# Kernel optimization log

Measured on AMD Instinct MI355X. Metric: run time of the kernel, lower is better.

Reference implementation:

```python
import jax, jax.numpy as jnp
import numpy as np

ATOM_DIM = 128; RBF_DIM = 32; GEOM_HID = 128; SCAT = 64; OUT = 64; CUTOFF = 5.0
MAX_Z = 100; Z_EMB = 32; E_DIM = 32; PAIR_HID = 64
B = 16; N = 64; P = 8000; NE = 80


def _lin(key, i, o):
    kw, kb = jax.random.split(key)
    W = jax.random.normal(kw, (i, o), jnp.float32) / np.sqrt(i).astype(np.float32)
    b = jax.random.normal(kb, (o,), jnp.float32) * 0.01
    return W, b


def setup_inputs() -> dict:
    key = jax.random.key(0)
    ks = jax.random.split(key, 24)
    inp = {}
    inp["h_flat"] = jax.random.normal(ks[0], (B * N, ATOM_DIM), jnp.float32)
    inp["z_flat"] = jax.random.randint(ks[1], (B * N,), 0, MAX_Z + 1)
    inp["e_feat"] = jax.random.normal(ks[2], (NE, E_DIM), jnp.float32)
    inp["path_j"] = jax.random.randint(ks[3], (P,), 0, B * N)
    inp["path_k"] = jax.random.randint(ks[4], (P,), 0, B * N)
    # distances in (0, 1.2*cutoff) so some paths exceed the cutoff
    inp["path_r0j"] = jax.random.uniform(ks[5], (P,), jnp.float32, 0.1, 1.2 * CUTOFF)
    inp["path_r0k"] = jax.random.uniform(ks[6], (P,), jnp.float32, 0.1, 1.2 * CUTOFF)
    inp["path_rjk"] = jax.random.uniform(ks[7], (P,), jnp.float32, 0.1, 1.2 * CUTOFF)
    inp["path_cosangle"] = jax.random.uniform(ks[8], (P,), jnp.float32, -1.0, 1.0)
    inp["path_batch"] = jnp.sort(jax.random.randint(ks[9], (P,), 0, B))
    inp["bsz"] = B
    # params
    inp["z_emb"] = jax.random.normal(ks[10], (MAX_Z + 1, Z_EMB), jnp.float32)
    pe_in = 2 * Z_EMB + E_DIM
    inp["pe_w1"], inp["pe_b1"] = _lin(ks[11], pe_in, PAIR_HID)
    inp["pe_w2"], inp["pe_b2"] = _lin(ks[12], PAIR_HID, PAIR_HID)
    inp["pe_w3"], inp["pe_b3"] = _lin(ks[13], PAIR_HID, SCAT)
    gm_in = 2 * ATOM_DIM + 3 * RBF_DIM + 1
    inp["gm_w1"], inp["gm_b1"] = _lin(ks[14], gm_in, GEOM_HID)
    inp["gm_w2"], inp["gm_b2"] = _lin(ks[15], GEOM_HID, GEOM_HID)
    inp["gm_w3"], inp["gm_b3"] = _lin(ks[16], GEOM_HID, SCAT)
    inp["op_w1"], inp["op_b1"] = _lin(ks[17], SCAT, GEOM_HID)
    inp["op_w2"], inp["op_b2"] = _lin(ks[18], GEOM_HID, OUT)
    return inp


def _rbf(r):
    centers = jnp.linspace(0.0, CUTOFF, RBF_DIM)
    width = centers[1] - centers[0]
    return jnp.exp(-0.5 * ((r[..., None] - centers) / width) ** 2)


def _cutoff_fn(r):
    return 0.5 * (jnp.cos(jnp.pi * r / CUTOFF) + 1.0) * (r < CUTOFF)


def _mlp3(x, w1, b1, w2, b2, w3, b3):
    h = jax.nn.silu(x @ w1 + b1)
    h = jax.nn.silu(h @ w2 + b2)
    return h @ w3 + b3


def _mlp2(x, w1, b1, w2, b2):
    return jax.nn.silu(x @ w1 + b1) @ w2 + b2


def reference(h_flat, z_flat, e_feat, path_j, path_k, path_r0j, path_r0k,
              path_rjk, path_cosangle, path_batch, bsz, z_emb,
              pe_w1, pe_b1, pe_w2, pe_b2, pe_w3, pe_b3,
              gm_w1, gm_b1, gm_w2, gm_b2, gm_w3, gm_b3,
              op_w1, op_b1, op_w2, op_b2):
    n_e = e_feat.shape[0]
    n_p = path_j.shape[0]
    # gather atom features
    hj = h_flat[path_j]                                  # (P, atom_dim)
    hk = h_flat[path_k]
    f0j = _rbf(jnp.minimum(path_r0j, CUTOFF))            # (P, rbf_dim)
    f0k = _rbf(jnp.minimum(path_r0k, CUTOFF))
    fjk = _rbf(jnp.minimum(path_rjk, CUTOFF))
    geom_in = jnp.concatenate([hj, hk, f0j, f0k, fjk, path_cosangle[:, None]], axis=-1)
    g_geom = _mlp3(geom_in, gm_w1, gm_b1, gm_w2, gm_b2, gm_w3, gm_b3)  # (P, scat)
    # element-pair energy features
    ej = z_emb[z_flat[path_j]]                           # (P, z_emb)
    ek = z_emb[z_flat[path_k]]
    pair_in = jnp.concatenate([
        jnp.broadcast_to(ej[:, None, :], (n_p, n_e, ej.shape[-1])),
        jnp.broadcast_to(ek[:, None, :], (n_p, n_e, ek.shape[-1])),
        jnp.broadcast_to(e_feat[None, :, :], (n_p, n_e, e_feat.shape[-1])),
    ], axis=-1)                                          # (P, nE, 2*z_emb+e_dim)
    g_elem = _mlp3(pair_in, pe_w1, pe_b1, pe_w2, pe_b2, pe_w3, pe_b3)  # (P, nE, scat)
    # cutoff weights and outer-product contribution
    cw = _cutoff_fn(path_r0j) * _cutoff_fn(path_r0k) * _cutoff_fn(path_rjk)  # (P,)
    contrib = g_geom[:, None, :] * g_elem * cw[:, None, None]          # (P, nE, scat)
    # scatter-add into batch bins
    agg = jax.ops.segment_sum(contrib, path_batch, num_segments=bsz)   # (B, nE, scat)
    norm = jax.ops.segment_sum(cw, path_batch, num_segments=bsz)       # (B,)
    agg = agg / jnp.maximum(norm, 1e-8)[:, None, None]
    return _mlp2(agg, op_w1, op_b1, op_w2, op_b2)                      # (B, nE, out)
```

## Files before the change

### kernel.cpp

```cpp
#include <hip/hip_runtime.h>
#include <math.h>

typedef float f32x4 __attribute__((ext_vector_type(4)));
typedef short bf16x8 __attribute__((ext_vector_type(8)));
typedef unsigned short u16;

#define RBF_DIM 32
#define CUTOFF 5.0f
#define PI_F 3.14159265358979323846f
#define BB 16
#define PP 8000
#define NEE 80

#define CW_OFF      0
#define GCW_OFF     8000
#define AGG_OFF     520000
#define ZEJW_OFF    601920
#define ZEKW_OFF    608384
#define EFWB_OFF    614848
#define NORM_OFF    619968
#define AIDX_OFF    619984
#define ZJA_OFF     627984
#define ZKA_OFF     635984
#define BOFF_OFF    643984
#define BCNT_OFF    644004
#define BSUM_OFF    644036
#define BCNTB_OFF   644548
#define BLKOFF_OFF  645060
#define CHS_OFF     645096
#define CHC_OFF     645362
#define CHB_OFF     645628
#define NC_OFF      645894
#define W2THI_OFF   645896
#define W2TLO_OFF   647944
#define W3THI_OFF   649992
#define W3TLO_OFF   652040
#define PJA_OFF     654088
#define PKA_OFF     662088
#define CWA_OFF     670088
#define HHI_OFF     678088
#define HLO_OFF     743624
#define GW1JKH_OFF  809160
#define GW1JKL_OFF  825544
#define GW1RH_OFF   841928
#define GW1RL_OFF   850120
#define GW2H_OFF    858312
#define GW2L_OFF    866504
#define GW3H_OFF    874696
#define GW3L_OFF    878792
#define HJW_OFF     882888
#define HKW_OFF     1013960

__device__ __forceinline__ float siluf(float x) { return x / (1.f + __expf(-x)); }
__device__ __forceinline__ float cutoff_fn(float r) {
    return (r < CUTOFF) ? 0.5f * (cosf(PI_F * r / CUTOFF) + 1.f) : 0.f;
}
__device__ __forceinline__ float rbff(float r, int i) {
    r = fminf(r, CUTOFF);
    float a = r * (31.0f / CUTOFF) - (float)i;
    return __expf(-0.5f * a * a);
}
__device__ __forceinline__ u16 f2bf_rne(float x) {
    unsigned u = __float_as_uint(x);
    return (u16)((u + 0x7FFFu + ((u >> 16) & 1u)) >> 16);
}
__device__ __forceinline__ unsigned cvtpk2(float a, float b) {
    unsigned r;
    asm("v_cvt_pk_bf16_f32 %0, %1, %2" : "=v"(r) : "v"(a), "v"(b));
    return r;
}
__device__ __forceinline__ void splitpack8(const float* xs, bf16x8& hi, bf16x8& lo) {
    union { bf16x8 v; unsigned u[4]; } H, L;
    #pragma unroll
    for (int d = 0; d < 4; ++d) {
        float a = xs[2 * d], b = xs[2 * d + 1];
        unsigned h = cvtpk2(a, b);
        float ra = a - __uint_as_float(h << 16);
        float rb = b - __uint_as_float(h & 0xFFFF0000u);
        H.u[d] = h;
        L.u[d] = cvtpk2(ra, rb);
    }
    hi = H.v; lo = L.v;
}

__global__ __launch_bounds__(256) void k0a_k1(
    const float* r0j, const float* r0k, const float* rjk, const int* pbatch,
    const float* z_emb, const float* e_feat, const float* pe_w1, const float* pe_b1,
    const float* pe_w2, const float* pe_w3,
    const float* h_flat, const float* gm_w1, const float* gm_w2, const float* gm_w3,
    float* ws, int* wsi)
{
    __shared__ float cwL[256];
    __shared__ int bL[256];
    __shared__ int redC[256];
    __shared__ float embL[4 * 32];
    int blkAll = blockIdx.x, t = threadIdx.x;
    if (blkAll < 32) {
        int bi = blkAll;
        for (int i = t; i < 2560; i += 256) ws[AGG_OFF + bi*2560 + i] = 0.f;
        int p = bi*250 + t;
        float cw = 0.f; int bin = -1; int valid = 0;
        if (t < 250) {
            cw = cutoff_fn(r0j[p]) * cutoff_fn(r0k[p]) * cutoff_fn(rjk[p]);
            ws[CW_OFF + p] = cw;
            bin = pbatch[p];
            valid = (cw > 0.f) ? 1 : 0;
        }
        cwL[t] = cw; bL[t] = bin; redC[t] = valid;
        __syncthreads();
        if (t < 16) {
            float s = 0.f; int c2 = 0;
            for (int i = 0; i < 256; ++i) {
                bool m = (bL[i] == t);
                s += m ? cwL[i] : 0.f;
                c2 += (m && cwL[i] > 0.f) ? 1 : 0;
            }
            ws[BSUM_OFF + bi*16 + t] = s;
            wsi[BCNTB_OFF + bi*16 + t] = c2;
        }
        __syncthreads();
        for (int s = 128; s > 0; s >>= 1) {
            if (t < s) redC[t] += redC[t + s];
            __syncthreads();
        }
        if (t == 0) wsi[BCNT_OFF + bi] = redC[0];
        return;
    }
    if (blkAll >= 106) {
        int blk = blkAll - 106;
        if (blk < 32) {
            u16* hh = (u16*)(ws + HHI_OFF);
            u16* hl = (u16*)(ws + HLO_OFF);
            int base = blk * 4096;
            for (int idx = t; idx < 4096; idx += 256) {
                int e = base + idx;
                float v = h_flat[e];
                u16 h = f2bf_rne(v);
                hh[e] = h;
                hl[e] = f2bf_rne(v - __uint_as_float(((unsigned)h) << 16));
            }
        } else if (blk < 34) {
            u16* wh = (u16*)(ws + GW1JKH_OFF);
            u16* wl = (u16*)(ws + GW1JKL_OFF);
            int base = (blk - 32) * 16384;
            for (int idx = t; idx < 16384; idx += 256) {
                int e = base + idx;
                int m = e >> 7, k = e & 127;
                float v = gm_w1[((m < 128) ? k : (128 + k)) * 128 + (m & 127)];
                u16 h = f2bf_rne(v);
                wh[e] = h;
                wl[e] = f2bf_rne(v - __uint_as_float(((unsigned)h) << 16));
            }
        } else if (blk == 34) {
            u16* wh = (u16*)(ws + GW1RH_OFF);
            u16* wl = (u16*)(ws + GW1RL_OFF);
            for (int e = t; e < 16384; e += 256) {
                int m = e >> 7, k = e & 127;
                float v = (k < 97) ? gm_w1[(256 + k) * 128 + m] : 0.f;
                u16 h = f2bf_rne(v);
                wh[e] = h;
                wl[e] = f2bf_rne(v - __uint_as_float(((unsigned)h) << 16));
            }
        } else if (blk == 35) {
            u16* wh = (u16*)(ws + GW2H_OFF);
            u16* wl = (u16*)(ws + GW2L_OFF);
            for (int e = t; e < 16384; e += 256) {
                int m = e >> 7, k = e & 127;
                float v = gm_w2[k * 128 + m];
                u16 h = f2bf_rne(v);
                wh[e] = h;
                wl[e] = f2bf_rne(v - __uint_as_float(((unsigned)h) << 16));
            }
        } else {
            u16* wh = (u16*)(ws + GW3H_OFF);
            u16* wl = (u16*)(ws + GW3L_OFF);
            for (int e = t; e < 8192; e += 256) {
                int m = e >> 7, k = e & 127;
                float v = gm_w3[k * 64 + m];
                u16 h = f2bf_rne(v);
                wh[e] = h;
                wl[e] = f2bf_rne(v - __uint_as_float(((unsigned)h) << 16));
            }
        }
        return;
    }
    int blk = blkAll - 32;
    if (blk >= 72) {
        const float* W = (blk == 72) ? pe_w2 : pe_w3;
        u16* hiD = (u16*)(ws + ((blk == 72) ? W2THI_OFF : W3THI_OFF));
        u16* loD = (u16*)(ws + ((blk == 72) ? W2TLO_OFF : W3TLO_OFF));
        for (int idx = t; idx < 4096; idx += 256) {
            int k = idx >> 6, n = idx & 63;
            float v = W[idx];
            u16 h = f2bf_rne(v);
            float hf = __uint_as_float(((unsigned)h) << 16);
            hiD[n*64 + k] = h;
            loD[n*64 + k] = f2bf_rne(v - hf);
        }
        return;
    }
    int r0, nrows, wbase;
    const float* src;
    float* dst;
    bool addb = false;
    if (blk < 26)      { r0 = blk * 4;        nrows = 101; src = z_emb;  wbase = 0;  dst = ws + ZEJW_OFF; }
    else if (blk < 52) { r0 = (blk - 26) * 4; nrows = 101; src = z_emb;  wbase = 32; dst = ws + ZEKW_OFF; }
    else               { r0 = (blk - 52) * 4; nrows = NEE; src = e_feat; wbase = 64; dst = ws + EFWB_OFF; addb = true; }
    if (t < 128) {
        int rl = t >> 5, i = t & 31;
        int r = r0 + rl;
        embL[t] = (r < nrows) ? src[r * 32 + i] : 0.f;
    }
    __syncthreads();
    int rl = t >> 6, c = t & 63;
    float acc = addb ? pe_b1[c] : 0.f;
    #pragma unroll
    for (int i = 0; i < 32; ++i)
        acc = fmaf(embL[rl * 32 + i], pe_w1[(wbase + i) * 64 + c], acc);
    int r = r0 + rl;
    if (r < nrows) dst[r * 64 + c] = acc;
}

__global__ __launch_bounds__(64) void k0b(float* ws, int* wsi)
{
    int t = threadIdx.x;
    if (t < 16) {
        float s = 0.f;
        for (int bi = 0; bi < 32; ++bi) s += ws[BSUM_OFF + bi*16 + t];
        ws[NORM_OFF + t] = s;
    }
    if (t == 0) {
        int off = 0;
        for (int bi = 0; bi < 32; ++bi) { wsi[BLKOFF_OFF + bi] = off; off += wsi[BCNT_OFF + bi]; }
        wsi[BLKOFF_OFF + 32] = off;
        int bs = 0;
        for (int b = 0; b < 16; ++b) {
            wsi[BOFF_OFF + b] = bs;
            int cb = 0;
            for (int bi = 0; bi < 32; ++bi) cb += wsi[BCNTB_OFF + bi*16 + b];
            bs += cb;
        }
        wsi[BOFF_OFF + 16] = bs;
        int nc = 0;
        for (int b = 0; b < 16; ++b) {
            int s0 = wsi[BOFF_OFF + b], e0 = wsi[BOFF_OFF + b + 1];
            for (int x = s0; x < e0; x += 32) {
                wsi[CHS_OFF + nc] = x;
                wsi[CHC_OFF + nc] = (e0 - x < 32) ? (e0 - x) : 32;
                wsi[CHB_OFF + nc] = b;
                nc++;
            }
        }
        wsi[NC_OFF] = nc;
    }
}

__global__ __launch_bounds__(256) void k0c(
    const int* pj, const int* pk, const int* zf, float* ws, int* wsi)
{
    __shared__ int sc[256];
    int bi = blockIdx.x, t = threadIdx.x;
    int p = bi*250 + t;
    int valid = (t < 250 && ws[CW_OFF + p] > 0.f) ? 1 : 0;
    sc[t] = valid;
    __syncthreads();
    for (int off = 1; off < 256; off <<= 1) {
        int v = (t >= off) ? sc[t - off] : 0;
        __syncthreads();
        sc[t] += v;
        __syncthreads();
    }
    if (valid) {
        int pos = wsi[BLKOFF_OFF + bi] + sc[t] - 1;
        int pjv = pj[p], pkv = pk[p];
        wsi[AIDX_OFF + pos] = p;
        wsi[ZJA_OFF + pos] = zf[pjv];
        wsi[ZKA_OFF + pos] = zf[pkv];
        wsi[PJA_OFF + pos] = pjv;
        wsi[PKA_OFF + pos] = pkv;
        ws[CWA_OFF + pos] = ws[CW_OFF + p];
    }
}

__global__ __launch_bounds__(256) void k1b_hw(float* ws)
{
    int t = threadIdx.x;
    int a0 = blockIdx.x * 64;
    int lane = t & 63, w = t >> 6, c = lane & 15, g = lane >> 4;
    const u16* hh = (const u16*)(ws + HHI_OFF);
    const u16* hl = (const u16*)(ws + HLO_OFF);
    const u16* wh = (const u16*)(ws + GW1JKH_OFF);
    const u16* wl = (const u16*)(ws + GW1JKL_OFF);
    f32x4 acc[4][4];
    #pragma unroll
    for (int i = 0; i < 4; ++i)
        #pragma unroll
        for (int j = 0; j < 4; ++j) acc[i][j] = (f32x4){0.f, 0.f, 0.f, 0.f};
    #pragma unroll 1
    for (int ks = 0; ks < 4; ++ks) {
        bf16x8 Ah[4], Al[4], Bh[4], Bl[4];
        #pragma unroll
        for (int mt = 0; mt < 4; ++mt) {
            int off = (w * 64 + mt * 16 + c) * 128 + ks * 32 + g * 8;
            Ah[mt] = *(const bf16x8*)(wh + off);
            Al[mt] = *(const bf16x8*)(wl + off);
        }
        #pragma unroll
        for (int nt = 0; nt < 4; ++nt) {
            int off = (a0 + nt * 16 + c) * 128 + ks * 32 + g * 8;
            Bh[nt] = *(const bf16x8*)(hh + off);
            Bl[nt] = *(const bf16x8*)(hl + off);
        }
        #pragma unroll
        for (int mt = 0; mt < 4; ++mt)
            #pragma unroll
            for (int nt = 0; nt < 4; ++nt) {
                f32x4 d = acc[mt][nt];
                d = __builtin_amdgcn_mfma_f32_16x16x32_bf16(Ah[mt], Bh[nt], d, 0, 0, 0);
                d = __builtin_amdgcn_mfma_f32_16x16x32_bf16(Ah[mt], Bl[nt], d, 0, 0, 0);
                d = __builtin_amdgcn_mfma_f32_16x16x32_bf16(Al[mt], Bh[nt], d, 0, 0, 0);
                acc[mt][nt] = d;
            }
    }
    float* dst = ws + ((w < 2) ? HJW_OFF : HKW_OFF);
    #pragma unroll
    for (int mt = 0; mt < 4; ++mt)
        #pragma unroll
        for (int nt = 0; nt < 4; ++nt) {
            int m = (w & 1) * 64 + mt * 16 + g * 4;
            int a = a0 + nt * 16 + c;
            *(f32x4*)(dst + a * 128 + m) = acc[mt][nt];
        }
}

__global__ __launch_bounds__(256) void k2_geom_mfma(
    const float* r0jG, const float* r0kG, const float* rjkG, const float* cosG,
    const float* b1g, const float* b2g, const float* b3g,
    float* ws, const int* wsi, float* gcw)
{
    __shared__ __align__(16) float sum3L[32 * 128];
    __shared__ __align__(16) u16 rbfH[4096], rbfL[4096];
    __shared__ __align__(16) u16 h1H[4096], h1L[4096];
    __shared__ __align__(16) u16 h2H[4096], h2L[4096];
    __shared__ int pjS[32], pkS[32];
    __shared__ float cwS[32], r0jS[32], r0kS[32], rjkS[32], cosS[32];

    int NC = wsi[NC_OFF];
    int cid = blockIdx.x;
    if (cid >= NC) return;
    int cs = wsi[CHS_OFF + cid], cnt = wsi[CHC_OFF + cid];
    int t = threadIdx.x, lane = t & 63, w = t >> 6, c = lane & 15, g = lane >> 4;

    if (t < 32) {
        int ap = cs + min(t, cnt - 1);
        int a = wsi[AIDX_OFF + ap];
        pjS[t] = wsi[PJA_OFF + ap]; pkS[t] = wsi[PKA_OFF + ap];
        cwS[t] = ws[CWA_OFF + ap];
        r0jS[t] = r0jG[a]; r0kS[t] = r0kG[a]; rjkS[t] = rjkG[a]; cosS[t] = cosG[a];
    }
    __syncthreads();
    {
        int p = t >> 3, kc = (t & 7) * 16;
        const float* rj = ws + HJW_OFF + pjS[p] * 128 + kc;
        const float* rk = ws + HKW_OFF + pkS[p] * 128 + kc;
        #pragma unroll
        for (int q = 0; q < 4; ++q) {
            f32x4 v = *(const f32x4*)(rj + q * 4) + *(const f32x4*)(rk + q * 4);
            *(f32x4*)(sum3L + ((p * 128 + kc + q * 4) ^ ((p & 7) << 2))) = v;
        }
    }
    {
        int p = t >> 3, k0 = (t & 7) * 16;
        float r0jv = r0jS[p], r0kv = r0kS[p], rjkv = rjkS[p], cv = cosS[p];
        #pragma unroll
        for (int hf = 0; hf < 2; ++hf) {
            int kb = k0 + hf * 8;
            float xs[8];
            #pragma unroll
            for (int i = 0; i < 8; ++i) {
                int k = kb + i;
                float v;
                if (k < 32) v = rbff(r0jv, k);
                else if (k < 64) v = rbff(r0kv, k - 32);
                else if (k < 96) v = rbff(rjkv, k - 64);
                else if (k == 96) v = cv;
                else v = 0.f;
                xs[i] = v;
            }
            bf16x8 hi, lo;
            splitpack8(xs, hi, lo);
            int idx = (p * 128 + kb) ^ ((p & 7) << 3);
            *(bf16x8*)(rbfH + idx) = hi;
            *(bf16x8*)(rbfL + idx) = lo;
        }
    }
    __syncthreads();

    const u16* w1h = (const u16*)(ws + GW1RH_OFF);
    const u16* w1l = (const u16*)(ws + GW1RL_OFF);
    const u16* w2h = (const u16*)(ws + GW2H_OFF);
    const u16* w2l = (const u16*)(ws + GW2L_OFF);
    const u16* w3h = (const u16*)(ws + GW3H_OFF);
    const u16* w3l = (const u16*)(ws + GW3L_OFF);

    f32x4 acc[2][2];
    #pragma unroll
    for (int i = 0; i < 2; ++i)
        #pragma unroll
        for (int j = 0; j < 2; ++j) acc[i][j] = (f32x4){0.f, 0.f, 0.f, 0.f};
    #pragma unroll 1
    for (int ks = 0; ks < 4; ++ks) {
        bf16x8 Ah[2], Al[2], Bh[2], Bl[2];
        #pragma unroll
        for (int ml = 0; ml < 2; ++ml) {
            int off = ((w * 2 + ml) * 16 + c) * 128 + ks * 32 + g * 8;
            Ah[ml] = *(const bf16x8*)(w1h + off);
            Al[ml] = *(const bf16x8*)(w1l + off);
        }
        #pragma unroll
        for (int nt = 0; nt < 2; ++nt) {
            int p = nt * 16 + c;
            int idx = (p * 128 + ks * 32 + g * 8) ^ ((p & 7) << 3);
            Bh[nt] = *(const bf16x8*)(rbfH + idx);
            Bl[nt] = *(const bf16x8*)(rbfL + idx);
        }
        #pragma unroll
        for (int ml = 0; ml < 2; ++ml)
            #pragma unroll
            for (int nt = 0; nt < 2; ++nt) {
                f32x4 d = acc[ml][nt];
                d = __builtin_amdgcn_mfma_f32_16x16x32_bf16(Ah[ml], Bh[nt], d, 0, 0, 0);
                d = __builtin_amdgcn_mfma_f32_16x16x32_bf16(Ah[ml], Bl[nt], d, 0, 0, 0);
                d = __builtin_amdgcn_mfma_f32_16x16x32_bf16(Al[ml], Bh[nt], d, 0, 0, 0);
                acc[ml][nt] = d;
            }
    }
    #pragma unroll
    for (int ml = 0; ml < 2; ++ml)
        #pragma unroll
        for (int nt = 0; nt < 2; ++nt) {
            int p = nt * 16 + c;
            int m0 = (w * 2 + ml) * 16 + g * 4;
            f32x4 s = *(const f32x4*)(sum3L + ((p * 128 + m0) ^ ((p & 7) << 2)));
            f32x4 bb = *(const f32x4*)(b1g + m0);
            f32x4 x = acc[ml][nt] + s + bb;
            float v0 = siluf(x[0]), v1 = siluf(x[1]), v2 = siluf(x[2]), v3 = siluf(x[3]);
            unsigned h01 = cvtpk2(v0, v1), h23 = cvtpk2(v2, v3);
            float l0 = v0 - __uint_as_float(h01 << 16);
            float l1 = v1 - __uint_as_float(h01 & 0xFFFF0000u);
            float l2 = v2 - __uint_as_float(h23 << 16);
            float l3 = v3 - __uint_as_float(h23 & 0xFFFF0000u);
            unsigned lo01 = cvtpk2(l0, l1), lo23 = cvtpk2(l2, l3);
            int idx = (p * 128 + m0) ^ ((p & 7) << 3);
            uint2 uh; uh.x = h01; uh.y = h23;
            uint2 ul; ul.x = lo01; ul.y = lo23;
            *(uint2*)(h1H + idx) = uh;
            *(uint2*)(h1L + idx) = ul;
        }
    __syncthreads();

    #pragma unroll
    for (int i = 0; i < 2; ++i)
        #pragma unroll
        for (int j = 0; j < 2; ++j) acc[i][j] = (f32x4){0.f, 0.f, 0.f, 0.f};
    #pragma unroll 1
    for (int ks = 0; ks < 4; ++ks) {
        bf16x8 Ah[2], Al[2], Bh[2], Bl[2];
        #pragma unroll
        for (int ml = 0; ml < 2; ++ml) {
            int off = ((w * 2 + ml) * 16 + c) * 128 + ks * 32 + g * 8;
            Ah[ml] = *(const bf16x8*)(w2h + off);
            Al[ml] = *(const bf16x8*)(w2l + off);
        }
        #pragma unroll
        for (int nt = 0; nt < 2; ++nt) {
            int p = nt * 16 + c;
            int idx = (p * 128 + ks * 32 + g * 8) ^ ((p & 7) << 3);
            Bh[nt] = *(const bf16x8*)(h1H + idx);
            Bl[nt] = *(const bf16x8*)(h1L + idx);
        }
        #pragma unroll
        for (int ml = 0; ml < 2; ++ml)
            #pragma unroll
            for (int nt = 0; nt < 2; ++nt) {
                f32x4 d = acc[ml][nt];
                d = __builtin_amdgcn_mfma_f32_16x16x32_bf16(Ah[ml], Bh[nt], d, 0, 0, 0);
                d = __builtin_amdgcn_mfma_f32_16x16x32_bf16(Ah[ml], Bl[nt], d, 0, 0, 0);
                d = __builtin_amdgcn_mfma_f32_16x16x32_bf16(Al[ml], Bh[nt], d, 0, 0, 0);
                acc[ml][nt] = d;
            }
    }
    #pragma unroll
    for (int ml = 0; ml < 2; ++ml)
        #pragma unroll
        for (int nt = 0; nt < 2; ++nt) {
            int p = nt * 16 + c;
            int m0 = (w * 2 + ml) * 16 + g * 4;
            f32x4 bb = *(const f32x4*)(b2g + m0);
            f32x4 x = acc[ml][nt] + bb;
            float v0 = siluf(x[0]), v1 = siluf(x[1]), v2 = siluf(x[2]), v3 = siluf(x[3]);
            unsigned h01 = cvtpk2(v0, v1), h23 = cvtpk2(v2, v3);
            float l0 = v0 - __uint_as_float(h01 << 16);
            float l1 = v1 - __uint_as_float(h01 & 0xFFFF0000u);
            float l2 = v2 - __uint_as_float(h23 << 16);
            float l3 = v3 - __uint_as_float(h23 & 0xFFFF0000u);
            unsigned lo01 = cvtpk2(l0, l1), lo23 = cvtpk2(l2, l3);
            int idx = (p * 128 + m0) ^ ((p & 7) << 3);
            uint2 uh; uh.x = h01; uh.y = h23;
            uint2 ul; ul.x = lo01; ul.y = lo23;
            *(uint2*)(h2H + idx) = uh;
            *(uint2*)(h2L + idx) = ul;
        }
    __syncthreads();

    f32x4 acc3[2];
    acc3[0] = (f32x4){0.f, 0.f, 0.f, 0.f};
    acc3[1] = (f32x4){0.f, 0.f, 0.f, 0.f};
    #pragma unroll 1
    for (int ks = 0; ks < 4; ++ks) {
        bf16x8 Ah, Al, Bh[2], Bl[2];
        {
            int off = (w * 16 + c) * 128 + ks * 32 + g * 8;
            Ah = *(const bf16x8*)(w3h + off);
            Al = *(const bf16x8*)(w3l + off);
        }
        #pragma unroll
        for (int nt = 0; nt < 2; ++nt) {
            int p = nt * 16 + c;
            int idx = (p * 128 + ks * 32 + g * 8) ^ ((p & 7) << 3);
            Bh[nt] = *(const bf16x8*)(h2H + idx);
            Bl[nt] = *(const bf16x8*)(h2L + idx);
        }
        #pragma unroll
        for (int nt = 0; nt < 2; ++nt) {
            f32x4 d = acc3[nt];
            d = __builtin_amdgcn_mfma_f32_16x16x32_bf16(Ah, Bh[nt], d, 0, 0, 0);
            d = __builtin_amdgcn_mfma_f32_16x16x32_bf16(Ah, Bl[nt], d, 0, 0, 0);
            d = __builtin_amdgcn_mfma_f32_16x16x32_bf16(Al, Bh[nt], d, 0, 0, 0);
            acc3[nt] = d;
        }
    }
    {
        int m0 = w * 16 + g * 4;
        f32x4 bb = *(const f32x4*)(b3g + m0);
        #pragma unroll
        for (int nt = 0; nt < 2; ++nt) {
            int p = nt * 16 + c;
            if (p < cnt) {
                f32x4 o = (acc3[nt] + bb) * cwS[p];
                *(f32x4*)(gcw + (cs + p) * 64 + m0) = o;
            }
        }
    }
}

__global__ __launch_bounds__(256) void k3_pair_mfma(
    const float* ws, const int* wsi, const float* gcw, float* agg,
    const float* b2g, const float* b3g)
{
    __shared__ __align__(16) float sL[32 * 64];
    __shared__ __align__(16) float gcwL[32 * 64];
    __shared__ __align__(16) u16 h2buf[4][4096];

    int NC = wsi[NC_OFF];
    int bid = blockIdx.x;
    int cid = bid / 5;
    int et  = bid - cid * 5;
    if (cid >= NC) return;
    int cs  = wsi[CHS_OFF + cid];
    int cnt = wsi[CHC_OFF + cid];
    int bb  = wsi[CHB_OFF + cid];

    int t = threadIdx.x;
    int lane = t & 63, w = t >> 6;
    int c = lane & 15, g = lane >> 4;

    {
        int p = t >> 3, kc = (t & 7) * 8;
        int ap = cs + min(p, cnt - 1);
        int zj = wsi[ZJA_OFF + ap], zk = wsi[ZKA_OFF + ap];
        const f32x4* rj = (const f32x4*)(ws + ZEJW_OFF + zj * 64 + kc);
        const f32x4* rk = (const f32x4*)(ws + ZEKW_OFF + zk * 64 + kc);
        f32x4 s0 = rj[0] + rk[0];
        f32x4 s1 = rj[1] + rk[1];
        int sw = (p & 7) << 2;
        *(f32x4*)(sL + ((p * 64 + kc) ^ sw))     = s0;
        *(f32x4*)(sL + ((p * 64 + kc + 4) ^ sw)) = s1;
        f32x4 g0 = {0.f, 0.f, 0.f, 0.f}, g1 = {0.f, 0.f, 0.f, 0.f};
        if (p < cnt) {
            g0 = *(const f32x4*)(gcw + (cs + p) * 64 + kc);
            g1 = *(const f32x4*)(gcw + (cs + p) * 64 + kc + 4);
        }
        *(f32x4*)(gcwL + ((p * 64 + kc) ^ sw))     = g0;
        *(f32x4*)(gcwL + ((p * 64 + kc + 4) ^ sw)) = g1;
    }

    const u16* w2hi = (const u16*)(ws + W2THI_OFF);
    const u16* w2lo = (const u16*)(ws + W2TLO_OFF);
    const u16* w3hi = (const u16*)(ws + W3THI_OFF);
    const u16* w3lo = (const u16*)(ws + W3TLO_OFF);
    bf16x8 A2h[4][2], A2l[4][2], A3h[4][2], A3l[4][2];
    #pragma unroll
    for (int mt = 0; mt < 4; ++mt)
        #pragma unroll
        for (int ks = 0; ks < 2; ++ks) {
            int off = (mt * 16 + c) * 64 + ks * 32 + g * 8;
            A2h[mt][ks] = *(const bf16x8*)(w2hi + off);
            A2l[mt][ks] = *(const bf16x8*)(w2lo + off);
            A3h[mt][ks] = *(const bf16x8*)(w3hi + off);
            A3l[mt][ks] = *(const bf16x8*)(w3lo + off);
        }
    f32x4 b2f[4], b3f[4];
    #pragma unroll
    for (int mt = 0; mt < 4; ++mt) {
        b2f[mt] = *(const f32x4*)(b2g + mt * 16 + 4 * g);
        b3f[mt] = *(const f32x4*)(b3g + mt * 16 + 4 * g);
    }
    __syncthreads();

    u16* myh = h2buf[w];
    u16* myl = h2buf[w] + 2048;
    float* red = (float*)h2buf[w];
    const float* efp = ws + EFWB_OFF;

    #pragma unroll 1
    for (int ei = 0; ei < 4; ++ei) {
        int e = et * 16 + w * 4 + ei;
        bf16x8 Bh[2][2], Bl[2][2];
        #pragma unroll
        for (int ks = 0; ks < 2; ++ks) {
            f32x4 e0 = *(const f32x4*)(efp + e * 64 + ks * 32 + g * 8);
            f32x4 e1 = *(const f32x4*)(efp + e * 64 + ks * 32 + g * 8 + 4);
            #pragma unroll
            for (int nt = 0; nt < 2; ++nt) {
                int p = nt * 16 + c;
                int sw = (p & 7) << 2;
                int base = p * 64 + ks * 32 + g * 8;
                f32x4 x0 = *(const f32x4*)(sL + (base ^ sw));
                f32x4 x1 = *(const f32x4*)(sL + ((base + 4) ^ sw));
                x0 += e0; x1 += e1;
                float xs[8];
                #pragma unroll
                for (int i = 0; i < 4; ++i) { xs[i] = siluf(x0[i]); xs[4 + i] = siluf(x1[i]); }
                splitpack8(xs, Bh[nt][ks], Bl[nt][ks]);
            }
        }
        f32x4 acc[4][2];
        #pragma unroll
        for (int mt = 0; mt < 4; ++mt)
            #pragma unroll
            for (int nt = 0; nt < 2; ++nt) {
                f32x4 d = {0.f, 0.f, 0.f, 0.f};
                #pragma unroll
                for (int ks = 0; ks < 2; ++ks) {
                    d = __builtin_amdgcn_mfma_f32_16x16x32_bf16(A2h[mt][ks], Bh[nt][ks], d, 0, 0, 0);
                    d = __builtin_amdgcn_mfma_f32_16x16x32_bf16(A2h[mt][ks], Bl[nt][ks], d, 0, 0, 0);
                    d = __builtin_amdgcn_mfma_f32_16x16x32_bf16(A2l[mt][ks], Bh[nt][ks], d, 0, 0, 0);
                }
                acc[mt][nt] = d;
            }
        #pragma unroll
        for (int mt = 0; mt < 4; ++mt)
            #pragma unroll
            for (int nt = 0; nt < 2; ++nt) {
                f32x4 h = acc[mt][nt] + b2f[mt];
                float v0 = siluf(h[0]), v1 = siluf(h[1]), v2 = siluf(h[2]), v3 = siluf(h[3]);
                unsigned h01 = cvtpk2(v0, v1), h23 = cvtpk2(v2, v3);
                float l0 = v0 - __uint_as_float(h01 << 16);
                float l1 = v1 - __uint_as_float(h01 & 0xFFFF0000u);
                float l2 = v2 - __uint_as_float(h23 << 16);
                float l3 = v3 - __uint_as_float(h23 & 0xFFFF0000u);
                unsigned lo01 = cvtpk2(l0, l1), lo23 = cvtpk2(l2, l3);
                int p = nt * 16 + c;
                int idx = (p * 64 + mt * 16 + 4 * g) ^ ((p & 7) << 3);
                uint2 uh, ul;
                uh.x = h01; uh.y = h23;
                ul.x = lo01; ul.y = lo23;
                *(uint2*)(myh + idx) = uh;
                *(uint2*)(myl + idx) = ul;
            }
        bf16x8 Ch[2][2], Cl[2][2];
        #pragma unroll
        for (int nt = 0; nt < 2; ++nt)
            #pragma unroll
            for (int ks = 0; ks < 2; ++ks) {
                int p = nt * 16 + c;
                int idx = (p * 64 + ks * 32 + g * 8) ^ ((p & 7) << 3);
                Ch[nt][ks] = *(const bf16x8*)(myh + idx);
                Cl[nt][ks] = *(const bf16x8*)(myl + idx);
            }
        #pragma unroll
        for (int mt = 0; mt < 4; ++mt)
            #pragma unroll
            for (int nt = 0; nt < 2; ++nt) {
                f32x4 d = {0.f, 0.f, 0.f, 0.f};
                #pragma unroll
                for (int ks = 0; ks < 2; ++ks) {
                    d = __builtin_amdgcn_mfma_f32_16x16x32_bf16(A3h[mt][ks], Ch[nt][ks], d, 0, 0, 0);
                    d = __builtin_amdgcn_mfma_f32_16x16x32_bf16(A3h[mt][ks], Cl[nt][ks], d, 0, 0, 0);
                    d = __builtin_amdgcn_mfma_f32_16x16x32_bf16(A3l[mt][ks], Ch[nt][ks], d, 0, 0, 0);
                }
                acc[mt][nt] = d;
            }
        float part[16];
        #pragma unroll
        for (int i = 0; i < 16; ++i) part[i] = 0.f;
        #pragma unroll
        for (int mt = 0; mt < 4; ++mt)
            #pragma unroll
            for (int nt = 0; nt < 2; ++nt) {
                f32x4 o = acc[mt][nt] + b3f[mt];
                int pl = nt * 16 + c;
                int gidx = (pl * 64 + mt * 16 + 4 * g) ^ ((pl & 7) << 2);
                f32x4 gv = *(const f32x4*)(gcwL + gidx);
                #pragma unroll
                for (int r = 0; r < 4; ++r) part[mt * 4 + r] += o[r] * gv[r];
            }
        #pragma unroll
        for (int i = 0; i < 16; ++i) {
            int mt = i >> 2, r = i & 3;
            red[(mt * 16 + g * 4 + r) * 17 + c] = part[i];
        }
        float s = 0.f;
        #pragma unroll
        for (int i = 0; i < 16; ++i) s += red[lane * 17 + i];
        atomicAdd(agg + (bb * NEE + e) * 64 + lane, s);
    }
}

__global__ __launch_bounds__(256) void k4_out(
    const float* ws, const float* W1, const float* b1,
    const float* W2, const float* b2, float* out)
{
    __shared__ float xT[64][68];
    __shared__ float W1L[64 * 128];
    __shared__ float hTT[128][68];
    __shared__ float W2L[128 * 64];
    __shared__ float normL[16];
    int t = threadIdx.x;
    int gbase = blockIdx.x * 64;
    if (t < 16) normL[t] = 1.f / fmaxf(ws[NORM_OFF + t], 1e-8f);
    for (int idx = t; idx < 8192; idx += 256) { W1L[idx] = W1[idx]; W2L[idx] = W2[idx]; }
    __syncthreads();
    {
        int r = t & 63, cq = t >> 6;
        int gg = gbase + r;
        int b = gg / NEE;
        float rn = normL[b];
        const float* arow = ws + AGG_OFF + gg * 64 + cq * 16;
        #pragma unroll
        for (int q = 0; q < 4; ++q) {
            float4 v = *(const float4*)(arow + q * 4);
            int c = cq * 16 + q * 4;
            xT[c + 0][r] = v.x * rn; xT[c + 1][r] = v.y * rn;
            xT[c + 2][r] = v.z * rn; xT[c + 3][r] = v.w * rn;
        }
    }
    __syncthreads();
    {
        int tcx = t & 15, trx = t >> 4;
        int c0 = tcx * 8, r0 = trx * 4;
        float acc[4][8];
        #pragma unroll
        for (int j = 0; j < 4; ++j)
            #pragma unroll
            for (int q = 0; q < 8; ++q) acc[j][q] = 0.f;
        #pragma unroll 4
        for (int kk = 0; kk < 64; ++kk) {
            float4 x4 = *(const float4*)&xT[kk][r0];
            float4 wa = *(const float4*)&W1L[kk * 128 + c0];
            float4 wb = *(const float4*)&W1L[kk * 128 + c0 + 4];
            float x[4] = {x4.x, x4.y, x4.z, x4.w};
            float w[8] = {wa.x, wa.y, wa.z, wa.w, wb.x, wb.y, wb.z, wb.w};
            #pragma unroll
            for (int j = 0; j < 4; ++j)
                #pragma unroll
                for (int q = 0; q < 8; ++q)
                    acc[j][q] = fmaf(x[j], w[q], acc[j][q]);
        }
        #pragma unroll
        for (int q = 0; q < 8; ++q) {
            float bb = b1[c0 + q];
            float4 v;
            v.x = siluf(acc[0][q] + bb);
            v.y = siluf(acc[1][q] + bb);
            v.z = siluf(acc[2][q] + bb);
            v.w = siluf(acc[3][q] + bb);
            *(float4*)&hTT[c0 + q][r0] = v;
        }
    }
    __syncthreads();
    {
        int tcx = t & 7, trx = t >> 3;
        int c0 = tcx * 8, r0 = trx * 2;
        float acc[2][8];
        #pragma unroll
        for (int j = 0; j < 2; ++j)
            #pragma unroll
            for (int q = 0; q < 8; ++q) acc[j][q] = 0.f;
        #pragma unroll 4
        for (int kk = 0; kk < 128; ++kk) {
            float2 x2 = *(const float2*)&hTT[kk][r0];
            float4 wa = *(const float4*)&W2L[kk * 64 + c0];
            float4 wb = *(const float4*)&W2L[kk * 64 + c0 + 4];
            float w[8] = {wa.x, wa.y, wa.z, wa.w, wb.x, wb.y, wb.z, wb.w};
            #pragma unroll
            for (int q = 0; q < 8; ++q) {
                acc[0][q] = fmaf(x2.x, w[q], acc[0][q]);
                acc[1][q] = fmaf(x2.y, w[q], acc[1][q]);
            }
        }
        int gg = gbase + r0;
        #pragma unroll
        for (int j = 0; j < 2; ++j) {
            float o[8];
            #pragma unroll
            for (int q = 0; q < 8; ++q) o[q] = acc[j][q] + b2[c0 + q];
            *(float4*)&out[(gg + j) * 64 + c0] = make_float4(o[0], o[1], o[2], o[3]);
            *(float4*)&out[(gg + j) * 64 + c0 + 4] = make_float4(o[4], o[5], o[6], o[7]);
        }
    }
}

extern "C" void kernel_launch(void* const* d_in, const int* in_sizes, int n_in,
                              void* d_out, int out_size, void* d_ws, size_t ws_size,
                              hipStream_t stream) {
    (void)in_sizes; (void)n_in; (void)out_size; (void)ws_size;
    const float* h_flat = (const float*)d_in[0];
    const int*   z_flat = (const int*)d_in[1];
    const float* e_feat = (const float*)d_in[2];
    const int*   path_j = (const int*)d_in[3];
    const int*   path_k = (const int*)d_in[4];
    const float* r0j    = (const float*)d_in[5];
    const float* r0k    = (const float*)d_in[6];
    const float* rjk    = (const float*)d_in[7];
    const float* cosang = (const float*)d_in[8];
    const int*   pbatch = (const int*)d_in[9];
    const float* z_emb  = (const float*)d_in[11];
    const float* pe_w1  = (const float*)d_in[12];
    const float* pe_b1  = (const float*)d_in[13];
    const float* pe_w2  = (const float*)d_in[14];
    const float* pe_b2  = (const float*)d_in[15];
    const float* pe_w3  = (const float*)d_in[16];
    const float* pe_b3  = (const float*)d_in[17];
    const float* gm_w1  = (const float*)d_in[18];
    const float* gm_b1  = (const float*)d_in[19];
    const float* gm_w2  = (const float*)d_in[20];
    const float* gm_b2  = (const float*)d_in[21];
    const float* gm_w3  = (const float*)d_in[22];
    const float* gm_b3  = (const float*)d_in[23];
    const float* op_w1  = (const float*)d_in[24];
    const float* op_b1  = (const float*)d_in[25];
    const float* op_w2  = (const float*)d_in[26];
    const float* op_b2  = (const float*)d_in[27];

    float* ws  = (float*)d_ws;
    int*   wsi = (int*)d_ws;
    float* gcw = ws + GCW_OFF;
    float* agg = ws + AGG_OFF;

    hipLaunchKernelGGL(k0a_k1, dim3(143), dim3(256), 0, stream,
                       r0j, r0k, rjk, pbatch,
                       z_emb, e_feat, pe_w1, pe_b1, pe_w2, pe_w3,
                       h_flat, gm_w1, gm_w2, gm_w3, ws, wsi);
    hipLaunchKernelGGL(k0b, dim3(1), dim3(64), 0, stream, ws, wsi);
    hipLaunchKernelGGL(k0c, dim3(32), dim3(256), 0, stream,
                       path_j, path_k, z_flat, ws, wsi);
    hipLaunchKernelGGL(k1b_hw, dim3(16), dim3(256), 0, stream, ws);
    hipLaunchKernelGGL(k2_geom_mfma, dim3(266), dim3(256), 0, stream,
                       r0j, r0k, rjk, cosang,
                       gm_b1, gm_b2, gm_b3, ws, wsi, gcw);
    hipLaunchKernelGGL(k3_pair_mfma, dim3(1330), dim3(256), 0, stream,
                       ws, wsi, gcw, agg, pe_b2, pe_b3);
    hipLaunchKernelGGL(k4_out, dim3(20), dim3(256), 0, stream,
                       ws, op_w1, op_b1, op_w2, op_b2, (float*)d_out);
}
```

Measured before the change: 148.3 us.

## Parallelize chunk setup, fuse compaction with hw GEMM, slim pair kernel registers

The single-thread scan in k0b is replaced by a parallel prefix sum and a parallel chunk table build. The compaction kernel and the h·W GEMM kernel are merged into one launch by splitting on block index. The pair MLP kernel moves its low-part weight fragments into swizzled LDS, restructures its MFMA loops to hold fewer live fragments, reads gcw straight from global instead of staging it in LDS, replaces the LDS reduction with wave shuffles, and sets launch bounds to aim for 4 blocks per CU. The aim is higher occupancy and less serial setup, at the cost of extra LDS reads and uncached global gcw loads in the inner loop.

Measured after the change: 182.9 us. +23.3%, slower.

```diff
diff --git a/kernel.cpp b/kernel.cpp
--- a/kernel.cpp
+++ b/kernel.cpp
@@ -221,71 +221,89 @@
     if (r < nrows) dst[r * 64 + c] = acc;
 }
 
-__global__ __launch_bounds__(64) void k0b(float* ws, int* wsi)
+__global__ __launch_bounds__(256) void k0b(float* ws, int* wsi)
 {
+    __shared__ int bcntL[32];
+    __shared__ int cntB[16];
+    __shared__ int boff[17];
+    __shared__ int chkoff[17];
     int t = threadIdx.x;
     if (t < 16) {
         float s = 0.f;
+        #pragma unroll 4
         for (int bi = 0; bi < 32; ++bi) s += ws[BSUM_OFF + bi*16 + t];
         ws[NORM_OFF + t] = s;
     }
+    if (t >= 32 && t < 48) {
+        int b = t - 32;
+        int cb = 0;
+        #pragma unroll 4
+        for (int bi = 0; bi < 32; ++bi) cb += wsi[BCNTB_OFF + bi*16 + b];
+        cntB[b] = cb;
+    }
+    if (t >= 64 && t < 96) bcntL[t - 64] = wsi[BCNT_OFF + (t - 64)];
+    __syncthreads();
+    for (int off = 1; off < 32; off <<= 1) {
+        int v = (t < 32 && t >= off) ? bcntL[t - off] : 0;
+        __syncthreads();
+        if (t < 32) bcntL[t] += v;
+        __syncthreads();
+    }
+    if (t < 32) wsi[BLKOFF_OFF + t] = bcntL[t] - wsi[BCNT_OFF + t];
     if (t == 0) {
-        int off = 0;
-        for (int bi = 0; bi < 32; ++bi) { wsi[BLKOFF_OFF + bi] = off; off += wsi[BCNT_OFF + bi]; }
-        wsi[BLKOFF_OFF + 32] = off;
-        int bs = 0;
+        wsi[BLKOFF_OFF + 32] = bcntL[31];
+        int bo = 0, co = 0;
         for (int b = 0; b < 16; ++b) {
-            wsi[BOFF_OFF + b] = bs;
-            int cb = 0;
-            for (int bi = 0; bi < 32; ++bi) cb += wsi[BCNTB_OFF + bi*16 + b];
-            bs += cb;
-        }
-        wsi[BOFF_OFF + 16] = bs;
-        int nc = 0;
-        for (int b = 0; b < 16; ++b) {
-            int s0 = wsi[BOFF_OFF + b], e0 = wsi[BOFF_OFF + b + 1];
-            for (int x = s0; x < e0; x += 32) {
-                wsi[CHS_OFF + nc] = x;
-                wsi[CHC_OFF + nc] = (e0 - x < 32) ? (e0 - x) : 32;
-                wsi[CHB_OFF + nc] = b;
-                nc++;
-            }
-        }
-        wsi[NC_OFF] = nc;
-    }
-}
-
-__global__ __launch_bounds__(256) void k0c(
+            boff[b] = bo; chkoff[b] = co;
+            bo += cntB[b];
+            co += (cntB[b] + 31) >> 5;
+        }
+        boff[16] = bo; chkoff[16] = co;
+        wsi[NC_OFF] = co;
+    }
+    __syncthreads();
+    int NCv = chkoff[16];
+    for (int ci = t; ci < NCv; ci += 256) {
+        int b = 0;
+        while (chkoff[b + 1] <= ci) b++;
+        int local = ci - chkoff[b];
+        int rem = cntB[b] - local * 32;
+        wsi[CHS_OFF + ci] = boff[b] + local * 32;
+        wsi[CHC_OFF + ci] = (rem < 32) ? rem : 32;
+        wsi[CHB_OFF + ci] = b;
+    }
+}
+
+__global__ __launch_bounds__(256) void k0c_k1b(
     const int* pj, const int* pk, const int* zf, float* ws, int* wsi)
 {
     __shared__ int sc[256];
-    int bi = blockIdx.x, t = threadIdx.x;
-    int p = bi*250 + t;
-    int valid = (t < 250 && ws[CW_OFF + p] > 0.f) ? 1 : 0;
-    sc[t] = valid;
-    __syncthreads();
-    for (int off = 1; off < 256; off <<= 1) {
-        int v = (t >= off) ? sc[t - off] : 0;
+    int blk = blockIdx.x, t = threadIdx.x;
+    if (blk < 32) {
+        int bi = blk;
+        int p = bi*250 + t;
+        int valid = (t < 250 && ws[CW_OFF + p] > 0.f) ? 1 : 0;
+        sc[t] = valid;
         __syncthreads();
-        sc[t] += v;
-        __syncthreads();
-    }
-    if (valid) {
-        int pos = wsi[BLKOFF_OFF + bi] + sc[t] - 1;
-        int pjv = pj[p], pkv = pk[p];
-        wsi[AIDX_OFF + pos] = p;
-        wsi[ZJA_OFF + pos] = zf[pjv];
-        wsi[ZKA_OFF + pos] = zf[pkv];
-        wsi[PJA_OFF + pos] = pjv;
-        wsi[PKA_OFF + pos] = pkv;
-        ws[CWA_OFF + pos] = ws[CW_OFF + p];
-    }
-}
-
-__global__ __launch_bounds__(256) void k1b_hw(float* ws)
-{
-    int t = threadIdx.x;
-    int a0 = blockIdx.x * 64;
+        for (int off = 1; off < 256; off <<= 1) {
+            int v = (t >= off) ? sc[t - off] : 0;
+            __syncthreads();
+            sc[t] += v;
+            __syncthreads();
+        }
+        if (valid) {
+            int pos = wsi[BLKOFF_OFF + bi] + sc[t] - 1;
+            int pjv = pj[p], pkv = pk[p];
+            wsi[AIDX_OFF + pos] = p;
+            wsi[ZJA_OFF + pos] = zf[pjv];
+            wsi[ZKA_OFF + pos] = zf[pkv];
+            wsi[PJA_OFF + pos] = pjv;
+            wsi[PKA_OFF + pos] = pkv;
+            ws[CWA_OFF + pos] = ws[CW_OFF + p];
+        }
+        return;
+    }
+    int a0 = (blk - 32) * 64;
     int lane = t & 63, w = t >> 6, c = lane & 15, g = lane >> 4;
     const u16* hh = (const u16*)(ws + HHI_OFF);
     const u16* hl = (const u16*)(ws + HLO_OFF);
@@ -554,13 +572,14 @@
     }
 }
 
-__global__ __launch_bounds__(256) void k3_pair_mfma(
+__global__ __launch_bounds__(256, 4) void k3_pair_mfma(
     const float* ws, const int* wsi, const float* gcw, float* agg,
     const float* b2g, const float* b3g)
 {
     __shared__ __align__(16) float sL[32 * 64];
-    __shared__ __align__(16) float gcwL[32 * 64];
-    __shared__ __align__(16) u16 h2buf[4][4096];
+    __shared__ __align__(16) u16 h2buf[4][2048];
+    __shared__ __align__(16) u16 a2lL[4096];
+    __shared__ __align__(16) u16 a3lL[4096];
 
     int NC = wsi[NC_OFF];
     int bid = blockIdx.x;
@@ -581,56 +600,55 @@
         int zj = wsi[ZJA_OFF + ap], zk = wsi[ZKA_OFF + ap];
         const f32x4* rj = (const f32x4*)(ws + ZEJW_OFF + zj * 64 + kc);
         const f32x4* rk = (const f32x4*)(ws + ZEKW_OFF + zk * 64 + kc);
-        f32x4 s0 = rj[0] + rk[0];
-        f32x4 s1 = rj[1] + rk[1];
         int sw = (p & 7) << 2;
-        *(f32x4*)(sL + ((p * 64 + kc) ^ sw))     = s0;
-        *(f32x4*)(sL + ((p * 64 + kc + 4) ^ sw)) = s1;
-        f32x4 g0 = {0.f, 0.f, 0.f, 0.f}, g1 = {0.f, 0.f, 0.f, 0.f};
-        if (p < cnt) {
-            g0 = *(const f32x4*)(gcw + (cs + p) * 64 + kc);
-            g1 = *(const f32x4*)(gcw + (cs + p) * 64 + kc + 4);
-        }
-        *(f32x4*)(gcwL + ((p * 64 + kc) ^ sw))     = g0;
-        *(f32x4*)(gcwL + ((p * 64 + kc + 4) ^ sw)) = g1;
-    }
-
+        *(f32x4*)(sL + ((p * 64 + kc) ^ sw))     = rj[0] + rk[0];
+        *(f32x4*)(sL + ((p * 64 + kc + 4) ^ sw)) = rj[1] + rk[1];
+    }
+    {
+        const unsigned* s2 = (const unsigned*)(ws + W2TLO_OFF);
+        const unsigned* s3 = (const unsigned*)(ws + W3TLO_OFF);
+        unsigned* d2 = (unsigned*)a2lL;
+        unsigned* d3 = (unsigned*)a3lL;
+        #pragma unroll
+        for (int rr = 0; rr < 8; ++rr) {
+            int i = rr * 256 + t;
+            int sw = ((i >> 5) & 7) << 2;
+            d2[i ^ sw] = s2[i];
+            d3[i ^ sw] = s3[i];
+        }
+    }
     const u16* w2hi = (const u16*)(ws + W2THI_OFF);
-    const u16* w2lo = (const u16*)(ws + W2TLO_OFF);
     const u16* w3hi = (const u16*)(ws + W3THI_OFF);
-    const u16* w3lo = (const u16*)(ws + W3TLO_OFF);
-    bf16x8 A2h[4][2], A2l[4][2], A3h[4][2], A3l[4][2];
+    bf16x8 A2h[4][2], A3h[4][2];
     #pragma unroll
     for (int mt = 0; mt < 4; ++mt)
         #pragma unroll
         for (int ks = 0; ks < 2; ++ks) {
             int off = (mt * 16 + c) * 64 + ks * 32 + g * 8;
             A2h[mt][ks] = *(const bf16x8*)(w2hi + off);
-            A2l[mt][ks] = *(const bf16x8*)(w2lo + off);
             A3h[mt][ks] = *(const bf16x8*)(w3hi + off);
-            A3l[mt][ks] = *(const bf16x8*)(w3lo + off);
-        }
-    f32x4 b2f[4], b3f[4];
-    #pragma unroll
-    for (int mt = 0; mt < 4; ++mt) {
-        b2f[mt] = *(const f32x4*)(b2g + mt * 16 + 4 * g);
-        b3f[mt] = *(const f32x4*)(b3g + mt * 16 + 4 * g);
-    }
+        }
     __syncthreads();
 
     u16* myh = h2buf[w];
-    u16* myl = h2buf[w] + 2048;
-    float* red = (float*)h2buf[w];
+    u16* myl = h2buf[w] + 1024;
     const float* efp = ws + EFWB_OFF;
+    const int aswz = (c & 7) << 3;
 
     #pragma unroll 1
     for (int ei = 0; ei < 4; ++ei) {
         int e = et * 16 + w * 4 + ei;
-        bf16x8 Bh[2][2], Bl[2][2];
+        f32x4 acc[4][2];
+        #pragma unroll
+        for (int mt = 0; mt < 4; ++mt) {
+            acc[mt][0] = (f32x4){0.f, 0.f, 0.f, 0.f};
+            acc[mt][1] = (f32x4){0.f, 0.f, 0.f, 0.f};
+        }
         #pragma unroll
         for (int ks = 0; ks < 2; ++ks) {
             f32x4 e0 = *(const f32x4*)(efp + e * 64 + ks * 32 + g * 8);
             f32x4 e1 = *(const f32x4*)(efp + e * 64 + ks * 32 + g * 8 + 4);
+            bf16x8 Bh[2], Bl[2];
             #pragma unroll
             for (int nt = 0; nt < 2; ++nt) {
                 int p = nt * 16 + c;
@@ -642,28 +660,30 @@
                 float xs[8];
                 #pragma unroll
                 for (int i = 0; i < 4; ++i) { xs[i] = siluf(x0[i]); xs[4 + i] = siluf(x1[i]); }
-                splitpack8(xs, Bh[nt][ks], Bl[nt][ks]);
-            }
-        }
-        f32x4 acc[4][2];
-        #pragma unroll
-        for (int mt = 0; mt < 4; ++mt)
-            #pragma unroll
-            for (int nt = 0; nt < 2; ++nt) {
-                f32x4 d = {0.f, 0.f, 0.f, 0.f};
+                splitpack8(xs, Bh[nt], Bl[nt]);
+            }
+            #pragma unroll
+            for (int mt = 0; mt < 4; ++mt) {
+                bf16x8 a2l = *(const bf16x8*)(a2lL + (((mt * 16 + c) * 64 + ks * 32 + g * 8) ^ aswz));
                 #pragma unroll
-                for (int ks = 0; ks < 2; ++ks) {
-                    d = __builtin_amdgcn_mfma_f32_16x16x32_bf16(A2h[mt][ks], Bh[nt][ks], d, 0, 0, 0);
-                    d = __builtin_amdgcn_mfma_f32_16x16x32_bf16(A2h[mt][ks], Bl[nt][ks], d, 0, 0, 0);
-                    d = __builtin_amdgcn_mfma_f32_16x16x32_bf16(A2l[mt][ks], Bh[nt][ks], d, 0, 0, 0);
+                for (int nt = 0; nt < 2; ++nt) {
+                    f32x4 d = acc[mt][nt];
+                    d = __builtin_amdgcn_mfma_f32_16x16x32_bf16(A2h[mt][ks], Bh[nt], d, 0, 0, 0);
+                    d = __builtin_amdgcn_mfma_f32_16x16x32_bf16(A2h[mt][ks], Bl[nt], d, 0, 0, 0);
+                    d = __builtin_amdgcn_mfma_f32_16x16x32_bf16(a2l,         Bh[nt], d, 0, 0, 0);
+                    acc[mt][nt] = d;
                 }
-                acc[mt][nt] = d;
-            }
-        #pragma unroll
-        for (int mt = 0; mt < 4; ++mt)
-            #pragma unroll
-            for (int nt = 0; nt < 2; ++nt) {
-                f32x4 h = acc[mt][nt] + b2f[mt];
+            }
+        }
+        float part[16];
+        #pragma unroll
+        for (int i = 0; i < 16; ++i) part[i] = 0.f;
+        #pragma unroll
+        for (int nt = 0; nt < 2; ++nt) {
+            #pragma unroll
+            for (int mt = 0; mt < 4; ++mt) {
+                f32x4 b2v = *(const f32x4*)(b2g + mt * 16 + 4 * g);
+                f32x4 h = acc[mt][nt] + b2v;
                 float v0 = siluf(h[0]), v1 = siluf(h[1]), v2 = siluf(h[2]), v3 = siluf(h[3]);
                 unsigned h01 = cvtpk2(v0, v1), h23 = cvtpk2(v2, v3);
                 float l0 = v0 - __uint_as_float(h01 << 16);
@@ -671,60 +691,51 @@
                 float l2 = v2 - __uint_as_float(h23 << 16);
                 float l3 = v3 - __uint_as_float(h23 & 0xFFFF0000u);
                 unsigned lo01 = cvtpk2(l0, l1), lo23 = cvtpk2(l2, l3);
-                int p = nt * 16 + c;
-                int idx = (p * 64 + mt * 16 + 4 * g) ^ ((p & 7) << 3);
+                int idx = (c * 64 + mt * 16 + 4 * g) ^ aswz;
                 uint2 uh, ul;
                 uh.x = h01; uh.y = h23;
                 ul.x = lo01; ul.y = lo23;
                 *(uint2*)(myh + idx) = uh;
                 *(uint2*)(myl + idx) = ul;
-            }
-        bf16x8 Ch[2][2], Cl[2][2];
-        #pragma unroll
-        for (int nt = 0; nt < 2; ++nt)
+                acc[mt][nt] = (f32x4){0.f, 0.f, 0.f, 0.f};
+            }
             #pragma unroll
             for (int ks = 0; ks < 2; ++ks) {
-                int p = nt * 16 + c;
-                int idx = (p * 64 + ks * 32 + g * 8) ^ ((p & 7) << 3);
-                Ch[nt][ks] = *(const bf16x8*)(myh + idx);
-                Cl[nt][ks] = *(const bf16x8*)(myl + idx);
-            }
-        #pragma unroll
-        for (int mt = 0; mt < 4; ++mt)
-            #pragma unroll
-            for (int nt = 0; nt < 2; ++nt) {
-                f32x4 d = {0.f, 0.f, 0.f, 0.f};
+                int idx = (c * 64 + ks * 32 + g * 8) ^ aswz;
+                bf16x8 Ch = *(const bf16x8*)(myh + idx);
+                bf16x8 Cl = *(const bf16x8*)(myl + idx);
                 #pragma unroll
-                for (int ks = 0; ks < 2; ++ks) {
-                    d = __builtin_amdgcn_mfma_f32_16x16x32_bf16(A3h[mt][ks], Ch[nt][ks], d, 0, 0, 0);
-                    d = __builtin_amdgcn_mfma_f32_16x16x32_bf16(A3h[mt][ks], Cl[nt][ks], d, 0, 0, 0);
-                    d = __builtin_amdgcn_mfma_f32_16x16x32_bf16(A3l[mt][ks], Ch[nt][ks], d, 0, 0, 0);
+                for (int mt = 0; mt < 4; ++mt) {
+                    bf16x8 a3l = *(const bf16x8*)(a3lL + (((mt * 16 + c) * 64 + ks * 32 + g * 8) ^ aswz));
+                    f32x4 d = acc[mt][nt];
+                    d = __builtin_amdgcn_mfma_f32_16x16x32_bf16(A3h[mt][ks], Ch, d, 0, 0, 0);
+                    d = __builtin_amdgcn_mfma_f32_16x16x32_bf16(A3h[mt][ks], Cl, d, 0, 0, 0);
+                    d = __builtin_amdgcn_mfma_f32_16x16x32_bf16(a3l,         Ch, d, 0, 0, 0);
+                    acc[mt][nt] = d;
                 }
-                acc[mt][nt] = d;
-            }
-        float part[16];
-        #pragma unroll
-        for (int i = 0; i < 16; ++i) part[i] = 0.f;
-        #pragma unroll
-        for (int mt = 0; mt < 4; ++mt)
-            #pragma unroll
-            for (int nt = 0; nt < 2; ++nt) {
-                f32x4 o = acc[mt][nt] + b3f[mt];
-                int pl = nt * 16 + c;
-                int gidx = (pl * 64 + mt * 16 + 4 * g) ^ ((pl & 7) << 2);
-                f32x4 gv = *(const f32x4*)(gcwL + gidx);
+            }
+            int pl = nt * 16 + c;
+            #pragma unroll
+            for (int mt = 0; mt < 4; ++mt) {
+                f32x4 b3v = *(const f32x4*)(b3g + mt * 16 + 4 * g);
+                f32x4 o = acc[mt][nt] + b3v;
+                f32x4 gv = (f32x4){0.f, 0.f, 0.f, 0.f};
+                if (pl < cnt) gv = *(const f32x4*)(gcw + (cs + pl) * 64 + mt * 16 + 4 * g);
                 #pragma unroll
                 for (int r = 0; r < 4; ++r) part[mt * 4 + r] += o[r] * gv[r];
             }
+        }
         #pragma unroll
         for (int i = 0; i < 16; ++i) {
-            int mt = i >> 2, r = i & 3;
-            red[(mt * 16 + g * 4 + r) * 17 + c] = part[i];
-        }
-        float s = 0.f;
-        #pragma unroll
-        for (int i = 0; i < 16; ++i) s += red[lane * 17 + i];
-        atomicAdd(agg + (bb * NEE + e) * 64 + lane, s);
+            float v = part[i];
+            v += __shfl_xor(v, 1, 64);
+            v += __shfl_xor(v, 2, 64);
+            v += __shfl_xor(v, 4, 64);
+            v += __shfl_xor(v, 8, 64);
+            part[i] = v;
+        }
+        int f = (c >> 2) * 16 + g * 4 + (c & 3);
+        atomicAdd(agg + (bb * NEE + e) * 64 + f, part[c]);
     }
 }
 
@@ -863,10 +874,9 @@
                        r0j, r0k, rjk, pbatch,
                        z_emb, e_feat, pe_w1, pe_b1, pe_w2, pe_w3,
                        h_flat, gm_w1, gm_w2, gm_w3, ws, wsi);
-    hipLaunchKernelGGL(k0b, dim3(1), dim3(64), 0, stream, ws, wsi);
-    hipLaunchKernelGGL(k0c, dim3(32), dim3(256), 0, stream,
+    hipLaunchKernelGGL(k0b, dim3(1), dim3(256), 0, stream, ws, wsi);
+    hipLaunchKernelGGL(k0c_k1b, dim3(48), dim3(256), 0, stream,
                        path_j, path_k, z_flat, ws, wsi);
-    hipLaunchKernelGGL(k1b_hw, dim3(16), dim3(256), 0, stream, ws);
     hipLaunchKernelGGL(k2_geom_mfma, dim3(266), dim3(256), 0, stream,
                        r0j, r0k, rjk, cosang,
                        gm_b1, gm_b2, gm_b3, ws, wsi, gcw);
```
